# Kernel tuning notes

Measured on AMD Instinct MI355X. Metric: run time of the kernel, lower is better.

## Reference

```python
import jax, jax.numpy as jnp
import numpy as np

N = 100_000          # nodes
E = 1_600_000        # edges (before self-loops)
D_NODE = 128
D_EDGE = 16
H1, C1 = 8, 8        # conv1: heads=8, out=8 -> concat dim 64
D_EMB = 64           # conv2: heads=1, out=embedding_dim, concat=False
NEG_SLOPE = 0.2      # GATv2 LeakyReLU slope (PyG default)


def _glorot(key, shape, fan):
    return jax.random.normal(key, shape, jnp.float32) * (1.0 / np.sqrt(fan))


def setup_inputs() -> dict:
    key = jax.random.key(0)
    ks = jax.random.split(key, 16)
    return {
        "x": jax.random.normal(ks[0], (N, D_NODE), jnp.float32),
        "edge_index": jax.random.randint(ks[1], (2, E), 0, N, jnp.int64),
        "edge_attr": jax.random.normal(ks[2], (E, D_EDGE), jnp.float32),
        # conv1 params
        "Wl1": _glorot(ks[3], (D_NODE, H1 * C1), D_NODE),
        "bl1": jnp.zeros((H1 * C1,), jnp.float32),
        "Wr1": _glorot(ks[4], (D_NODE, H1 * C1), D_NODE),
        "br1": jnp.zeros((H1 * C1,), jnp.float32),
        "We1": _glorot(ks[5], (D_EDGE, H1 * C1), D_EDGE),
        "att1": _glorot(ks[6], (H1, C1), C1),
        "b1": jnp.zeros((H1 * C1,), jnp.float32),
        # conv2 params (heads=1)
        "Wl2": _glorot(ks[7], (H1 * C1, D_EMB), H1 * C1),
        "bl2": jnp.zeros((D_EMB,), jnp.float32),
        "Wr2": _glorot(ks[8], (H1 * C1, D_EMB), H1 * C1),
        "br2": jnp.zeros((D_EMB,), jnp.float32),
        "We2": _glorot(ks[9], (D_EDGE, D_EMB), D_EDGE),
        "att2": _glorot(ks[10], (1, D_EMB), D_EMB),
        "b2": jnp.zeros((D_EMB,), jnp.float32),
    }


def _add_self_loops(edge_index, edge_attr, n):
    # PyG add_self_loops with fill_value='mean': self-loop edge_attr = mean of
    # incoming edge attrs per destination node.
    src, dst = edge_index[0], edge_index[1]
    ones = jnp.ones((src.shape[0],), edge_attr.dtype)
    deg = jax.ops.segment_sum(ones, dst, num_segments=n)
    ea_mean = jax.ops.segment_sum(edge_attr, dst, num_segments=n)
    ea_mean = ea_mean / jnp.maximum(deg, 1.0)[:, None]
    loop = jnp.arange(n, dtype=src.dtype)
    src2 = jnp.concatenate([src, loop])
    dst2 = jnp.concatenate([dst, loop])
    ea2 = jnp.concatenate([edge_attr, ea_mean], axis=0)
    return src2, dst2, ea2


def _segment_softmax(scores, seg, n):
    # scores: [E, H], seg: [E] destination-node ids
    m = jax.ops.segment_max(scores, seg, num_segments=n)
    m = jnp.where(jnp.isfinite(m), m, 0.0)          # empty segments -> 0
    e = jnp.exp(scores - m[seg])
    s = jax.ops.segment_sum(e, seg, num_segments=n)
    return e / (s[seg] + 1e-16)


def _gatv2(x, src, dst, ea, Wl, bl, Wr, br, We, att, bias, heads, ch, concat):
    n = x.shape[0]
    xl = (x @ Wl + bl).reshape(n, heads, ch)        # W_l x (messages)
    xr = (x @ Wr + br).reshape(n, heads, ch)        # W_r x (queries)
    ee = (ea @ We).reshape(-1, heads, ch)           # edge features
    z = jax.nn.leaky_relu(xl[src] + xr[dst] + ee, NEG_SLOPE)  # [E,H,C]
    score = jnp.einsum('ehc,hc->eh', z, att)
    alpha = _segment_softmax(score, dst, n)         # per-dst softmax
    out = jax.ops.segment_sum(xl[src] * alpha[:, :, None], dst, num_segments=n)
    out = out.reshape(n, heads * ch) if concat else out.mean(axis=1)
    return out + bias


def reference(x, edge_index, edge_attr,
              Wl1, bl1, Wr1, br1, We1, att1, b1,
              Wl2, bl2, Wr2, br2, We2, att2, b2):
    n = x.shape[0]
    src, dst, ea = _add_self_loops(edge_index, edge_attr, n)
    # dropout layers are no-ops in eval mode
    h = jax.nn.elu(_gatv2(x, src, dst, ea, Wl1, bl1, Wr1, br1, We1, att1, b1,
                          H1, C1, True))
    out = _gatv2(h, src, dst, ea, Wl2, bl2, Wr2, br2, We2, att2, b2,
                 1, D_EMB, False)
    return out
```

## Files before the change

kernel.cpp:

```cpp
#include <hip/hip_runtime.h>
#include <hip/hip_bf16.h>

typedef __hip_bfloat16 bf16;

struct Ptrs16 { const void* p[16]; };

__device__ __constant__ int wcnt[14] = {8192,64,8192,64,1024,64,64,4096,64,4096,64,1024,64,64};
__device__ __constant__ int woff[14] = {0,8192,8256,16448,16512,17536,17600,17664,21760,21824,25920,25984,27008,27072};
#define WTOTAL 27136

__global__ void detect_float(Ptrs16 ptrs, int n0, int n1, int* __restrict__ flags)
{
    int b = blockIdx.x, lane = threadIdx.x;
    int count = (b == 0) ? n0 : (b == 1) ? n1 : wcnt[b - 2];
    int limit = count < 1024 ? count : 1024;
    const unsigned short* us = (const unsigned short*)ptrs.p[b];
    int found = 0;
    for (int i = lane; i < limit; i += 64) {
        int e = (us[i] >> 7) & 0xFF;
        if (e >= 143) found = 1;
    }
    unsigned long long any = __ballot(found);
    if (lane == 0) flags[b] = (any != 0ull) ? 0 : 1;
}

__global__ void detect_idx(const int* __restrict__ ei, int* __restrict__ emode)
{
    if (threadIdx.x == 0) {
        int allz = 1;
        for (int i = 0; i < 128; i++)
            if (ei[2 * i + 1] != 0) { allz = 0; break; }
        emode[0] = allz;
    }
}

__global__ __launch_bounds__(256) void convert_weights(
    Ptrs16 ptrs, const int* __restrict__ flags, float* __restrict__ dst)
{
    int i = blockIdx.x * 256 + threadIdx.x;
    if (i >= WTOTAL) return;
    int r = 0;
    while (r < 13 && i >= woff[r + 1]) r++;
    int j = i - woff[r];
    const void* src = ptrs.p[2 + r];
    float v = flags[2 + r] ? __bfloat162float(((const bf16*)src)[j])
                           : ((const float*)src)[j];
    dst[i] = v;
}

__global__ __launch_bounds__(256) void count_kernel(
    const int* __restrict__ ei, int* __restrict__ deg,
    const int* __restrict__ emode, int E, int N)
{
    int e = blockIdx.x * 256 + threadIdx.x;
    if (e >= E) return;
    int stride = 1 + emode[0];
    int d = ei[(E + e) * stride];
    if ((unsigned)d >= (unsigned)N) d = 0;
    atomicAdd(&deg[d], 1);
}

__global__ __launch_bounds__(256) void scan1(
    const int* __restrict__ deg, int* __restrict__ rowptr,
    int* __restrict__ bsum, int N)
{
    __shared__ int ts[256];
    int b = blockIdx.x, t = threadIdx.x;
    int base = b * 1024 + t * 4;
    int v[4]; int s = 0;
#pragma unroll
    for (int i = 0; i < 4; i++) {
        int idx = base + i;
        v[i] = (idx < N) ? deg[idx] : 0;
        s += v[i];
    }
    ts[t] = s;
    __syncthreads();
    for (int off = 1; off < 256; off <<= 1) {
        int x = (t >= off) ? ts[t - off] : 0;
        __syncthreads();
        ts[t] += x;
        __syncthreads();
    }
    int run = (t == 0) ? 0 : ts[t - 1];
#pragma unroll
    for (int i = 0; i < 4; i++) {
        run += v[i];
        int idx = base + i;
        if (idx < N) rowptr[idx + 1] = run;
    }
    if (t == 255) bsum[b] = ts[255];
}

__global__ __launch_bounds__(256) void scan2(int* __restrict__ bsum, int nb)
{
    __shared__ int s[256];
    int t = threadIdx.x;
    s[t] = (t < nb) ? bsum[t] : 0;
    __syncthreads();
    for (int off = 1; off < 256; off <<= 1) {
        int v = (t >= off) ? s[t - off] : 0;
        __syncthreads();
        s[t] += v;
        __syncthreads();
    }
    if (t < nb) bsum[t] = (t == 0) ? 0 : s[t - 1];
}

__global__ __launch_bounds__(256) void scan3(
    int* __restrict__ rowptr, int* __restrict__ fill,
    const int* __restrict__ bsum, int N)
{
    int i = blockIdx.x * 256 + threadIdx.x;
    if (i > N) return;
    int v = (i == 0) ? 0 : rowptr[i] + bsum[(i - 1) >> 10];
    rowptr[i] = v;
    if (i < N) fill[i] = v;
}

__global__ __launch_bounds__(256) void scatter_kernel(
    const int* __restrict__ ei, int* __restrict__ fill,
    const float* __restrict__ ea, float* __restrict__ ea_csr,
    int* __restrict__ src_csr, const int* __restrict__ emode, int E, int N)
{
    int e = blockIdx.x * 256 + threadIdx.x;
    if (e >= E) return;
    int stride = 1 + emode[0];
    int d = ei[(E + e) * stride];
    int s = ei[e * stride];
    if ((unsigned)d >= (unsigned)N) d = 0;
    if ((unsigned)s >= (unsigned)N) s = 0;
    const float4* ea4 = (const float4*)ea;
    float4 v0 = ea4[(long)e * 4 + 0];
    float4 v1 = ea4[(long)e * 4 + 1];
    float4 v2 = ea4[(long)e * 4 + 2];
    float4 v3 = ea4[(long)e * 4 + 3];
    int pos = atomicAdd(&fill[d], 1);
    src_csr[pos] = s;
    float4* dst = (float4*)ea_csr + (long)pos * 4;
    dst[0] = v0; dst[1] = v1; dst[2] = v2; dst[3] = v3;
}

template<int K>
__global__ __launch_bounds__(256) void node_gemm(
    const float* __restrict__ X,
    const float* __restrict__ W0, const float* __restrict__ bias0, float* __restrict__ out0,
    const float* __restrict__ W1, const float* __restrict__ bias1, float* __restrict__ out1,
    int N)
{
    const float* W    = blockIdx.y ? W1 : W0;
    const float* bias = blockIdx.y ? bias1 : bias0;
    float* out        = blockIdx.y ? out1 : out0;

    __shared__ float Ws[K * 64];
    __shared__ float xs[4][4][K];

    for (int idx = threadIdx.x; idx < K * 64; idx += 256)
        Ws[idx] = W[idx];

    int wave = threadIdx.x >> 6, lane = threadIdx.x & 63;
    int r0 = blockIdx.x * 16 + wave * 4;
#pragma unroll
    for (int i = 0; i < 4; i++) {
        int r = r0 + i;
        for (int k = lane; k < K; k += 64)
            xs[wave][i][k] = (r < N) ? X[(long)r * K + k] : 0.0f;
    }
    __syncthreads();

    float a0 = 0.f, a1 = 0.f, a2 = 0.f, a3 = 0.f;
#pragma unroll 4
    for (int k = 0; k < K; k += 4) {
        float4 xv0 = *(const float4*)&xs[wave][0][k];
        float4 xv1 = *(const float4*)&xs[wave][1][k];
        float4 xv2 = *(const float4*)&xs[wave][2][k];
        float4 xv3 = *(const float4*)&xs[wave][3][k];
        float w0 = Ws[(k + 0) * 64 + lane];
        float w1 = Ws[(k + 1) * 64 + lane];
        float w2 = Ws[(k + 2) * 64 + lane];
        float w3 = Ws[(k + 3) * 64 + lane];
        a0 += xv0.x * w0; a1 += xv1.x * w0; a2 += xv2.x * w0; a3 += xv3.x * w0;
        a0 += xv0.y * w1; a1 += xv1.y * w1; a2 += xv2.y * w1; a3 += xv3.y * w1;
        a0 += xv0.z * w2; a1 += xv1.z * w2; a2 += xv2.z * w2; a3 += xv3.z * w2;
        a0 += xv0.w * w3; a1 += xv1.w * w3; a2 += xv2.w * w3; a3 += xv3.w * w3;
    }
    float bz = bias[lane];
    if (r0 + 0 < N) out[(long)(r0 + 0) * 64 + lane] = a0 + bz;
    if (r0 + 1 < N) out[(long)(r0 + 1) * 64 + lane] = a1 + bz;
    if (r0 + 2 < N) out[(long)(r0 + 2) * 64 + lane] = a2 + bz;
    if (r0 + 3 < N) out[(long)(r0 + 3) * 64 + lane] = a3 + bz;
}

#define DPP_ADD(t, ctrl)                                                      \
    t += __int_as_float(__builtin_amdgcn_update_dpp(                          \
             0, __float_as_int(t), (ctrl), 0xF, 0xF, true))

template<int CPH>
__device__ __forceinline__ float group_reduce(float t)
{
    if (CPH == 8) {
        DPP_ADD(t, 0xB1);
        DPP_ADD(t, 0x4E);
        t += __shfl_xor(t, 4, 64);
    } else {
        DPP_ADD(t, 0x111);
        DPP_ADD(t, 0x112);
        DPP_ADD(t, 0x114);
        DPP_ADD(t, 0x118);
        DPP_ADD(t, 0x142);
        DPP_ADD(t, 0x143);
        t = __int_as_float(__builtin_amdgcn_readlane(__float_as_int(t), 63));
    }
    return t;
}

template<int CPH, bool FINAL>
__global__ __launch_bounds__(256) void edge_kernel(
    const int* __restrict__ rowptr, const int* __restrict__ src_csr,
    const float* __restrict__ ea_csr,
    const float* __restrict__ xl, const float* __restrict__ xr,
    const float* __restrict__ We, const float* __restrict__ att,
    const float* __restrict__ bias, float* __restrict__ outp, int N)
{
    __shared__ float elds[4][256];

    int lane = threadIdx.x & 63;
    int wave = __builtin_amdgcn_readfirstlane(threadIdx.x >> 6);
    int n = blockIdx.x * 4 + wave;
    if (n >= N) return;

    float wcol[16];
#pragma unroll
    for (int k = 0; k < 16; k++) wcol[k] = We[k * 64 + lane];
    float attc = att[lane];
    float xrc  = xr[(unsigned)n * 64 + lane];

    int p0 = __builtin_amdgcn_readfirstlane(rowptr[n]);
    int p1 = __builtin_amdgcn_readfirstlane(rowptr[n + 1]);
    int deg = p1 - p0;

    float l0 = 0.f, acc0 = 0.f, ees0 = 0.f;
    float l1 = 0.f, acc1 = 0.f, ees1 = 0.f;

#define BODY(I, XS, LL, AC, EE_) do {                                        \
    if (cbase + (I) < p1) {                                                  \
        const float4* ep_ = (const float4*)(lb + (I) * 16);                  \
        float4 a0 = ep_[0], a1 = ep_[1], a2 = ep_[2], a3 = ep_[3];           \
        float xls = XS;                                                      \
        int pn_ = cbase + (I) + 8; pn_ = (pn_ <= pl) ? pn_ : pl;             \
        int sn_ = __builtin_amdgcn_readfirstlane(src_csr[pn_]);              \
        XS = xl[(unsigned)sn_ * 64 + lane];                                  \
        float t0 = a0.x*wcol[0]  + a0.y*wcol[1];                             \
        float t1 = a0.z*wcol[2]  + a0.w*wcol[3];                             \
        float t2 = a1.x*wcol[4]  + a1.y*wcol[5];                             \
        float t3 = a1.z*wcol[6]  + a1.w*wcol[7];                             \
        float t4 = a2.x*wcol[8]  + a2.y*wcol[9];                             \
        float t5 = a2.z*wcol[10] + a2.w*wcol[11];                            \
        float t6 = a3.x*wcol[12] + a3.y*wcol[13];                            \
        float t7 = a3.z*wcol[14] + a3.w*wcol[15];                            \
        float ee = ((t0 + t1) + (t2 + t3)) + ((t4 + t5) + (t6 + t7));        \
        EE_ += ee;                                                           \
        float z = xls + xrc + ee;                                            \
        z = (z > 0.f) ? z : 0.2f * z;                                        \
        float t = group_reduce<CPH>(z * attc);                               \
        float pe = __expf(t);                                                \
        LL += pe; AC += pe * xls;                                            \
    } } while (0)

    if (deg > 0) {
        const float4* ea4c = (const float4*)ea_csr;
        float* lb = &elds[wave][0];
        int pl = p1 - 1;

        float4 nxt = ea4c[(long)p0 * 4 + lane];
        int i1 = (p0 + 1 <= pl) ? p0 + 1 : pl;
        int i2 = (p0 + 2 <= pl) ? p0 + 2 : pl;
        int i3 = (p0 + 3 <= pl) ? p0 + 3 : pl;
        int i4 = (p0 + 4 <= pl) ? p0 + 4 : pl;
        int i5 = (p0 + 5 <= pl) ? p0 + 5 : pl;
        int i6 = (p0 + 6 <= pl) ? p0 + 6 : pl;
        int i7 = (p0 + 7 <= pl) ? p0 + 7 : pl;
        int s0 = __builtin_amdgcn_readfirstlane(src_csr[p0]);
        int s1 = __builtin_amdgcn_readfirstlane(src_csr[i1]);
        int s2 = __builtin_amdgcn_readfirstlane(src_csr[i2]);
        int s3 = __builtin_amdgcn_readfirstlane(src_csr[i3]);
        int s4 = __builtin_amdgcn_readfirstlane(src_csr[i4]);
        int s5 = __builtin_amdgcn_readfirstlane(src_csr[i5]);
        int s6 = __builtin_amdgcn_readfirstlane(src_csr[i6]);
        int s7 = __builtin_amdgcn_readfirstlane(src_csr[i7]);
        float x0 = xl[(unsigned)s0 * 64 + lane];
        float x1 = xl[(unsigned)s1 * 64 + lane];
        float x2 = xl[(unsigned)s2 * 64 + lane];
        float x3 = xl[(unsigned)s3 * 64 + lane];
        float x4 = xl[(unsigned)s4 * 64 + lane];
        float x5 = xl[(unsigned)s5 * 64 + lane];
        float x6 = xl[(unsigned)s6 * 64 + lane];
        float x7 = xl[(unsigned)s7 * 64 + lane];

        int nch = (deg + 15) >> 4;
        for (int ch = 0; ch < nch; ch++) {
            int cbase = p0 + (ch << 4);
            ((float4*)lb)[lane] = nxt;
            if (ch + 1 < nch)
                nxt = ea4c[(long)(cbase + 16) * 4 + lane];
#pragma unroll
            for (int g = 0; g < 2; g++) {
                BODY(g * 8 + 0, x0, l0, acc0, ees0);
                BODY(g * 8 + 1, x1, l1, acc1, ees1);
                BODY(g * 8 + 2, x2, l0, acc0, ees0);
                BODY(g * 8 + 3, x3, l1, acc1, ees1);
                BODY(g * 8 + 4, x4, l0, acc0, ees0);
                BODY(g * 8 + 5, x5, l1, acc1, ees1);
                BODY(g * 8 + 6, x6, l0, acc0, ees0);
                BODY(g * 8 + 7, x7, l1, acc1, ees1);
            }
        }
    }
#undef BODY

    float l = l0 + l1, acc = acc0 + acc1, eeacc = ees0 + ees1;

    {
        float eeS = (deg > 0) ? eeacc / (float)deg : 0.f;
        float xls = xl[(unsigned)n * 64 + lane];
        float z = xls + xrc + eeS;
        z = (z > 0.f) ? z : 0.2f * z;
        float t = group_reduce<CPH>(z * attc);
        float pe = __expf(t);
        l   += pe;
        acc += pe * xls;
    }

    float out = acc / (l + 1e-16f);
    float v = out + bias[lane];
    if (FINAL) {
        outp[(unsigned)n * 64 + lane] = v;
    } else {
        outp[(unsigned)n * 64 + lane] = (v > 0.f) ? v : (__expf(v) - 1.f);
    }
}

extern "C" void kernel_launch(void* const* d_in, const int* in_sizes, int n_in,
                              void* d_out, int out_size, void* d_ws, size_t ws_size,
                              hipStream_t stream)
{
    const int N = in_sizes[0] / 128;
    const int E = (in_sizes[1] >= 6000000) ? in_sizes[1] / 4 : in_sizes[1] / 2;

    const int*   ei = (const int*)  d_in[1];
    const float* x  = (const float*)d_in[0];
    const float* ea = (const float*)d_in[2];

    Ptrs16 ptrs;
    ptrs.p[0] = d_in[0];
    ptrs.p[1] = d_in[2];
    for (int i = 0; i < 14; i++) ptrs.p[2 + i] = d_in[3 + i];

    char* p = (char*)d_ws;
    auto carve = [&](size_t bytes) {
        char* r = p;
        p += (bytes + 255) & ~(size_t)255;
        return r;
    };
    int*   flags   = (int*)  carve(256);
    int*   emode   = (int*)  carve(256);
    float* wts     = (float*)carve((size_t)WTOTAL * 4);
    int*   deg     = (int*)  carve((size_t)N * 4);
    int*   rowptr  = (int*)  carve((size_t)(N + 1) * 4);
    int*   fill    = (int*)  carve((size_t)N * 4);
    int*   bsum    = (int*)  carve(1024);
    float* xl      = (float*)carve((size_t)N * 64 * 4);
    float* xr      = (float*)carve((size_t)N * 64 * 4);
    float* h       = (float*)carve((size_t)N * 64 * 4);
    float* ea_csr  = (float*)carve((size_t)(E + 32) * 16 * 4);
    int*   src_csr = (int*)  carve((size_t)(E + 32) * 4);
    (void)ws_size; (void)n_in; (void)out_size;

    const float* Wl1f  = wts + 0;     const float* bl1f = wts + 8192;
    const float* Wr1f  = wts + 8256;  const float* br1f = wts + 16448;
    const float* We1f  = wts + 16512; const float* att1f= wts + 17536;
    const float* b1f   = wts + 17600;
    const float* Wl2f  = wts + 17664; const float* bl2f = wts + 21760;
    const float* Wr2f  = wts + 21824; const float* br2f = wts + 25920;
    const float* We2f  = wts + 25984; const float* att2f= wts + 27008;
    const float* b2f   = wts + 27072;

    hipMemsetAsync(deg, 0, (size_t)N * 4, stream);

    detect_float<<<16, 64, 0, stream>>>(ptrs, in_sizes[0], in_sizes[2], flags);
    detect_idx<<<1, 64, 0, stream>>>(ei, emode);
    convert_weights<<<(WTOTAL + 255) / 256, 256, 0, stream>>>(ptrs, flags, wts);

    count_kernel<<<(E + 255) / 256, 256, 0, stream>>>(ei, deg, emode, E, N);

    int nb = (N + 1023) / 1024;
    scan1<<<nb, 256, 0, stream>>>(deg, rowptr, bsum, N);
    scan2<<<1, 256, 0, stream>>>(bsum, nb);
    scan3<<<(N + 256) / 256, 256, 0, stream>>>(rowptr, fill, bsum, N);

    scatter_kernel<<<(E + 255) / 256, 256, 0, stream>>>(
        ei, fill, ea, ea_csr, src_csr, emode, E, N);

    dim3 g1((N + 15) / 16, 2);
    node_gemm<128><<<g1, 256, 0, stream>>>(x, Wl1f, bl1f, xl, Wr1f, br1f, xr, N);
    int ng = (N + 3) / 4;
    edge_kernel<8, false><<<ng, 256, 0, stream>>>(
        rowptr, src_csr, ea_csr, xl, xr, We1f, att1f, b1f, h, N);

    node_gemm<64><<<g1, 256, 0, stream>>>(h, Wl2f, bl2f, xl, Wr2f, br2f, xr, N);
    edge_kernel<64, true><<<ng, 256, 0, stream>>>(
        rowptr, src_csr, ea_csr, xl, xr, We2f, att2f, b2f, (float*)d_out, N);
}
```

Measured before the change: 832.7 us.

## Load edge attrs via uniform broadcast registers instead of LDS staging; DPP reduce

Drops the per-wave LDS staging buffer for edge attributes. Each edge's 16 floats are now loaded straight into registers with wave-uniform addresses, prefetched four edges ahead in a rotating set of register buffers. The loop goes from 16-edge chunks to 8-edge iterations. It also replaces the shfl_xor(4) step in the 8-channel group reduction with two DPP row shifts and a per-lane select, avoiding the LDS-based ds_bpermute. This raises register pressure and issues four global loads per edge instead of one coalesced load per 16 edges.

```diff
diff --git a/kernel.cpp b/kernel.cpp
--- a/kernel.cpp
+++ b/kernel.cpp
@@ -195,13 +195,19 @@
     t += __int_as_float(__builtin_amdgcn_update_dpp(                          \
              0, __float_as_int(t), (ctrl), 0xF, 0xF, true))
 
+#define DPP_MOV(x, ctrl)                                                      \
+    __int_as_float(__builtin_amdgcn_update_dpp(                               \
+        0, __float_as_int(x), (ctrl), 0xF, 0xF, true))
+
 template<int CPH>
-__device__ __forceinline__ float group_reduce(float t)
+__device__ __forceinline__ float group_reduce(float t, bool hi4)
 {
     if (CPH == 8) {
         DPP_ADD(t, 0xB1);
         DPP_ADD(t, 0x4E);
-        t += __shfl_xor(t, 4, 64);
+        float up = DPP_MOV(t, 0x114);
+        float dn = DPP_MOV(t, 0x104);
+        t += hi4 ? up : dn;
     } else {
         DPP_ADD(t, 0x111);
         DPP_ADD(t, 0x112);
@@ -222,8 +228,6 @@
     const float* __restrict__ We, const float* __restrict__ att,
     const float* __restrict__ bias, float* __restrict__ outp, int N)
 {
-    __shared__ float elds[4][256];
-
     int lane = threadIdx.x & 63;
     int wave = __builtin_amdgcn_readfirstlane(threadIdx.x >> 6);
     int n = blockIdx.x * 4 + wave;
@@ -234,6 +238,7 @@
     for (int k = 0; k < 16; k++) wcol[k] = We[k * 64 + lane];
     float attc = att[lane];
     float xrc  = xr[(unsigned)n * 64 + lane];
+    bool hi4 = (lane & 4) != 0;
 
     int p0 = __builtin_amdgcn_readfirstlane(rowptr[n]);
     int p1 = __builtin_amdgcn_readfirstlane(rowptr[n + 1]);
@@ -242,13 +247,18 @@
     float l0 = 0.f, acc0 = 0.f, ees0 = 0.f;
     float l1 = 0.f, acc1 = 0.f, ees1 = 0.f;
 
-#define BODY(I, XS, LL, AC, EE_) do {                                        \
-    if (cbase + (I) < p1) {                                                  \
-        const float4* ep_ = (const float4*)(lb + (I) * 16);                  \
-        float4 a0 = ep_[0], a1 = ep_[1], a2 = ep_[2], a3 = ep_[3];           \
+#define BODY(J, EA_, XS, LL, AC, EE_) do {                                   \
+    if (p + (J) < p1) {                                                      \
+        float4 a0 = EA_##a, a1 = EA_##b, a2 = EA_##c, a3 = EA_##d;           \
         float xls = XS;                                                      \
-        int pn_ = cbase + (I) + 8; pn_ = (pn_ <= pl) ? pn_ : pl;             \
-        int sn_ = __builtin_amdgcn_readfirstlane(src_csr[pn_]);              \
+        int rp_ = p + (J) + 4; rp_ = (rp_ <= pl) ? rp_ : pl;                 \
+        rp_ = __builtin_amdgcn_readfirstlane(rp_);                           \
+        EA_##a = g4[(long)rp_ * 4 + 0];                                      \
+        EA_##b = g4[(long)rp_ * 4 + 1];                                      \
+        EA_##c = g4[(long)rp_ * 4 + 2];                                      \
+        EA_##d = g4[(long)rp_ * 4 + 3];                                      \
+        int xp_ = p + (J) + 8; xp_ = (xp_ <= pl) ? xp_ : pl;                 \
+        int sn_ = __builtin_amdgcn_readfirstlane(src_csr[xp_]);              \
         XS = xl[(unsigned)sn_ * 64 + lane];                                  \
         float t0 = a0.x*wcol[0]  + a0.y*wcol[1];                             \
         float t1 = a0.z*wcol[2]  + a0.w*wcol[3];                             \
@@ -262,32 +272,34 @@
         EE_ += ee;                                                           \
         float z = xls + xrc + ee;                                            \
         z = (z > 0.f) ? z : 0.2f * z;                                        \
-        float t = group_reduce<CPH>(z * attc);                               \
+        float t = group_reduce<CPH>(z * attc, hi4);                          \
         float pe = __expf(t);                                                \
         LL += pe; AC += pe * xls;                                            \
     } } while (0)
 
     if (deg > 0) {
-        const float4* ea4c = (const float4*)ea_csr;
-        float* lb = &elds[wave][0];
+        const float4* g4 = (const float4*)ea_csr;
         int pl = p1 - 1;
 
-        float4 nxt = ea4c[(long)p0 * 4 + lane];
-        int i1 = (p0 + 1 <= pl) ? p0 + 1 : pl;
-        int i2 = (p0 + 2 <= pl) ? p0 + 2 : pl;
-        int i3 = (p0 + 3 <= pl) ? p0 + 3 : pl;
-        int i4 = (p0 + 4 <= pl) ? p0 + 4 : pl;
-        int i5 = (p0 + 5 <= pl) ? p0 + 5 : pl;
-        int i6 = (p0 + 6 <= pl) ? p0 + 6 : pl;
-        int i7 = (p0 + 7 <= pl) ? p0 + 7 : pl;
-        int s0 = __builtin_amdgcn_readfirstlane(src_csr[p0]);
-        int s1 = __builtin_amdgcn_readfirstlane(src_csr[i1]);
-        int s2 = __builtin_amdgcn_readfirstlane(src_csr[i2]);
-        int s3 = __builtin_amdgcn_readfirstlane(src_csr[i3]);
-        int s4 = __builtin_amdgcn_readfirstlane(src_csr[i4]);
-        int s5 = __builtin_amdgcn_readfirstlane(src_csr[i5]);
-        int s6 = __builtin_amdgcn_readfirstlane(src_csr[i6]);
-        int s7 = __builtin_amdgcn_readfirstlane(src_csr[i7]);
+#define CL(K_) ((p0 + (K_) <= pl) ? p0 + (K_) : pl)
+        int q0 = CL(0), q1 = CL(1), q2 = CL(2), q3 = CL(3);
+        float4 E0a = g4[(long)q0*4+0], E0b = g4[(long)q0*4+1],
+               E0c = g4[(long)q0*4+2], E0d = g4[(long)q0*4+3];
+        float4 E1a = g4[(long)q1*4+0], E1b = g4[(long)q1*4+1],
+               E1c = g4[(long)q1*4+2], E1d = g4[(long)q1*4+3];
+        float4 E2a = g4[(long)q2*4+0], E2b = g4[(long)q2*4+1],
+               E2c = g4[(long)q2*4+2], E2d = g4[(long)q2*4+3];
+        float4 E3a = g4[(long)q3*4+0], E3b = g4[(long)q3*4+1],
+               E3c = g4[(long)q3*4+2], E3d = g4[(long)q3*4+3];
+        int s0 = __builtin_amdgcn_readfirstlane(src_csr[CL(0)]);
+        int s1 = __builtin_amdgcn_readfirstlane(src_csr[CL(1)]);
+        int s2 = __builtin_amdgcn_readfirstlane(src_csr[CL(2)]);
+        int s3 = __builtin_amdgcn_readfirstlane(src_csr[CL(3)]);
+        int s4 = __builtin_amdgcn_readfirstlane(src_csr[CL(4)]);
+        int s5 = __builtin_amdgcn_readfirstlane(src_csr[CL(5)]);
+        int s6 = __builtin_amdgcn_readfirstlane(src_csr[CL(6)]);
+        int s7 = __builtin_amdgcn_readfirstlane(src_csr[CL(7)]);
+#undef CL
         float x0 = xl[(unsigned)s0 * 64 + lane];
         float x1 = xl[(unsigned)s1 * 64 + lane];
         float x2 = xl[(unsigned)s2 * 64 + lane];
@@ -297,23 +309,15 @@
         float x6 = xl[(unsigned)s6 * 64 + lane];
         float x7 = xl[(unsigned)s7 * 64 + lane];
 
-        int nch = (deg + 15) >> 4;
-        for (int ch = 0; ch < nch; ch++) {
-            int cbase = p0 + (ch << 4);
-            ((float4*)lb)[lane] = nxt;
-            if (ch + 1 < nch)
-                nxt = ea4c[(long)(cbase + 16) * 4 + lane];
-#pragma unroll
-            for (int g = 0; g < 2; g++) {
-                BODY(g * 8 + 0, x0, l0, acc0, ees0);
-                BODY(g * 8 + 1, x1, l1, acc1, ees1);
-                BODY(g * 8 + 2, x2, l0, acc0, ees0);
-                BODY(g * 8 + 3, x3, l1, acc1, ees1);
-                BODY(g * 8 + 4, x4, l0, acc0, ees0);
-                BODY(g * 8 + 5, x5, l1, acc1, ees1);
-                BODY(g * 8 + 6, x6, l0, acc0, ees0);
-                BODY(g * 8 + 7, x7, l1, acc1, ees1);
-            }
+        for (int p = p0; p < p1; p += 8) {
+            BODY(0, E0, x0, l0, acc0, ees0);
+            BODY(1, E1, x1, l1, acc1, ees1);
+            BODY(2, E2, x2, l0, acc0, ees0);
+            BODY(3, E3, x3, l1, acc1, ees1);
+            BODY(4, E0, x4, l0, acc0, ees0);
+            BODY(5, E1, x5, l1, acc1, ees1);
+            BODY(6, E2, x6, l0, acc0, ees0);
+            BODY(7, E3, x7, l1, acc1, ees1);
         }
     }
 #undef BODY
@@ -325,7 +329,7 @@
         float xls = xl[(unsigned)n * 64 + lane];
         float z = xls + xrc + eeS;
         z = (z > 0.f) ? z : 0.2f * z;
-        float t = group_reduce<CPH>(z * attc);
+        float t = group_reduce<CPH>(z * attc, hi4);
         float pe = __expf(t);
         l   += pe;
         acc += pe * xls;
```

New measurement: 911.5 us. 9.5% more time.
